# Kernel tuning notes

Measured on AMD Instinct MI355X. Metric: run time of the kernel, lower is better.

Reference implementation:

```python
import jax, jax.numpy as jnp
import numpy as np
from math import factorial as _f

# ---------- Wigner 3j / real Clebsch-Gordan (numpy, build-time) ----------

def _w3j(j1, j2, j3, m1, m2, m3):
    if m1 + m2 + m3 != 0 or not (abs(j1 - j2) <= j3 <= j1 + j2):
        return 0.0
    t1, t2 = j2 - m1 - j3, j1 + m2 - j3
    t3, t4, t5 = j1 + j2 - j3, j1 - m1, j2 + m2
    s = 0.0
    for t in range(max(0, t1, t2), min(t3, t4, t5) + 1):
        s += (-1.0) ** t / (_f(t) * _f(t - t1) * _f(t - t2) * _f(t3 - t) * _f(t4 - t) * _f(t5 - t))
    n = ((-1.0) ** (j1 - j2 - m3)
         * (_f(j1 + j2 - j3) * _f(j1 - j2 + j3) * _f(-j1 + j2 + j3) / _f(j1 + j2 + j3 + 1)) ** 0.5
         * (_f(j1 + m1) * _f(j1 - m1) * _f(j2 + m2) * _f(j2 - m2) * _f(j3 + m3) * _f(j3 - m3)) ** 0.5)
    return n * s


def _Umat(l):
    # complex -> real spherical-harmonic basis change
    U = np.zeros((2 * l + 1, 2 * l + 1), dtype=complex)
    U[l, l] = 1.0
    s2 = 1.0 / np.sqrt(2.0)
    for m in range(1, l + 1):
        U[l + m, l + m] = (-1.0) ** m * s2
        U[l + m, l - m] = s2
        U[l - m, l - m] = 1j * s2
        U[l - m, l + m] = -1j * (-1.0) ** m * s2
    return U


def _real_cg(l1, l2, l3):
    Cc = np.zeros((2 * l1 + 1, 2 * l2 + 1, 2 * l3 + 1), dtype=complex)
    for m1 in range(-l1, l1 + 1):
        for m2 in range(-l2, l2 + 1):
            m3 = m1 + m2
            if abs(m3) <= l3:
                Cc[l1 + m1, l2 + m2, l3 + m3] = ((-1.0) ** (l1 - l2 + m3) * np.sqrt(2 * l3 + 1)
                                                 * _w3j(l1, l2, l3, m1, m2, -m3))
    C = np.einsum('am,bn,co,mno->abc', _Umat(l1), _Umat(l2), np.conj(_Umat(l3)), Cc)
    C = C.imag if np.abs(C.imag).sum() > np.abs(C.real).sum() else C.real
    C = C / np.sqrt((C ** 2).sum())  # w3j normalization
    return (C * np.sqrt(2 * l3 + 1)).astype(np.float32)  # component normalization

_TRIPLES = [(1, 1, 2), (1, 2, 3), (0, 0, 0), (1, 1, 0), (2, 2, 0),
            (0, 1, 1), (1, 0, 1), (1, 2, 1), (2, 1, 1), (3, 2, 1),
            (0, 2, 2), (2, 0, 2), (2, 2, 2), (3, 1, 2)]
_CG = {k: jnp.asarray(_real_cg(*k)) for k in _TRIPLES}

# tensor-product channel lists: (l_Y, l_V) pairs producing each output l (filter 0e+1o+2e)
_P_L0 = [(0, 0), (1, 1), (2, 2)]
_P_L1 = [(0, 1), (1, 0), (1, 2), (2, 1), (3, 2)]
_P_L2 = [(0, 2), (1, 1), (2, 0), (2, 2), (3, 1)]
_EPS = 0.1       # epsilon (~1/sqrt(avg_num_neighbors))
_ENV_P = 6       # polynomial envelope order


def _sph(u):
    # component-normalized real spherical harmonics l=0..3 of unit vectors u, m=-l..l order
    E = u.shape[0]
    y0 = jnp.ones((E, 1), u.dtype)
    y1 = np.float32(np.sqrt(3.0)) * u[:, jnp.array([1, 2, 0])]  # real l=1 basis (y,z,x)
    t2 = jnp.einsum('abc,ea,eb->ec', _CG[(1, 1, 2)], y1, y1)
    y2 = t2 * (np.float32(np.sqrt(5.0)) / jnp.linalg.norm(t2, axis=-1, keepdims=True))
    t3 = jnp.einsum('abc,ea,eb->ec', _CG[(1, 2, 3)], y1, y2)
    y3 = t3 * (np.float32(np.sqrt(7.0)) / jnp.linalg.norm(t3, axis=-1, keepdims=True))
    return jnp.concatenate([y0, y1, y2, y3], axis=-1)  # (E,16)


def _lin(h, W):
    return h @ (W / np.float32(np.sqrt(W.shape[0])))  # fan-in normalized linear


def _envelope(d):
    p = _ENV_P
    c1 = np.float32((p + 1) * (p + 2) / 2.0)
    c2 = np.float32(p * (p + 2))
    c3 = np.float32(p * (p + 1) / 2.0)
    f = 1.0 - c1 * d ** p + c2 * d ** (p + 1) - c3 * d ** (p + 2)
    return jnp.where(d < 1.0, f, 0.0)


def _forward(vectors, x, V, senders, n_nodes, W1, W2a, W2b, W2c, Wv1, Wv2):
    E = vectors.shape[0]
    lengths = jnp.linalg.norm(vectors, axis=-1)            # (E,)
    Y = _sph(vectors / lengths[:, None])                   # (E,16)
    w = _lin(x, W1)                                        # (E,64) edge weights
    wY = w[:, :, None] * Y[:, None, :]                     # (E,64,16)
    node = jax.ops.segment_sum(wY, senders, num_segments=n_nodes)
    wY = node[senders] * np.float32(_EPS)                  # scatter_sum with map_back
    A = {0: wY[..., 0:1], 1: wY[..., 1:4], 2: wY[..., 4:9], 3: wY[..., 9:16]}
    B = {0: V[..., 0:1], 1: V[..., 1:4], 2: V[..., 4:9]}

    def tp(pairs, l3):
        outs = [jnp.einsum('abc,eua,eub->euc', _CG[(l1, l2, l3)], A[l1], B[l2])
                for (l1, l2) in pairs]
        return jnp.stack(outs, axis=2)                     # (E,64,n_pairs,2l3+1)

    S = tp(_P_L0, 0).reshape(E, -1)                        # (E,192) 0e scalars -> join x
    V1 = tp(_P_L1, 1).reshape(E, -1, 3)                    # (E,320,3) 1o
    V2 = tp(_P_L2, 2).reshape(E, -1, 5)                    # (E,320,5) 2e

    x2 = jnp.concatenate([x, S], axis=1)                   # (E, d_x+192)
    h = jax.nn.silu(_lin(x2, W2a))
    h = jax.nn.silu(_lin(h, W2b))
    h = _lin(h, W2c)                                       # (E,64), no output act
    x_out = _envelope(lengths)[:, None] * h                # smoothing envelope

    V1o = jnp.einsum('euc,uk->ekc', V1, Wv1 / np.float32(np.sqrt(Wv1.shape[0])))  # (E,64,3)
    V2e = jnp.einsum('euc,uk->ekc', V2, Wv2 / np.float32(np.sqrt(Wv2.shape[0])))  # (E,64,5)
    V_out = jnp.concatenate([V1o.reshape(E, -1), V2e.reshape(E, -1)], axis=1)     # (E,512)
    return x_out, V_out


def setup_inputs() -> dict:
    key = jax.random.key(0)
    ks = jax.random.split(key, 12)
    E, N, DX, MUL = 32768, 2048, 128, 64
    vectors = jax.random.uniform(ks[0], (E, 3), jnp.float32) - 0.5  # |r| < 1 (inside cutoff)
    x = jax.random.normal(ks[1], (E, DX), jnp.float32)
    V = jax.random.normal(ks[2], (E, MUL, 9), jnp.float32)          # 64 slots x (0e+1o+2e)
    senders = jax.random.randint(ks[3], (E,), 0, N)
    species = jax.random.randint(ks[4], (N,), 0, 4, jnp.int32)
    W1 = jax.random.normal(ks[5], (DX, MUL), jnp.float32)
    W2a = jax.random.normal(ks[6], (DX + 192, 64), jnp.float32)
    W2b = jax.random.normal(ks[7], (64, 64), jnp.float32)
    W2c = jax.random.normal(ks[8], (64, 64), jnp.float32)
    Wv1 = jax.random.normal(ks[9], (320, 64), jnp.float32)
    Wv2 = jax.random.normal(ks[10], (320, 64), jnp.float32)
    return dict(vectors=vectors, x=x, V=V, senders=senders, species=species,
                W1=W1, W2a=W2a, W2b=W2b, W2c=W2c, Wv1=Wv1, Wv2=Wv2)


def reference(vectors, x, V, senders, species, W1, W2a, W2b, W2c, Wv1, Wv2):
    # species is unused by the layer body (matches original signature)
    return _forward(vectors, x, V, senders, int(species.shape[0]), W1, W2a, W2b, W2c, Wv1, Wv2)
```

## Files before the change

kernel.cpp:

```cpp
#include <hip/hip_runtime.h>
#include <cmath>
#include <complex>
#include <vector>
#include <algorithm>

namespace {

static double factd(int n) { double r = 1; for (int i = 2; i <= n; i++) r *= i; return r; }
static double par(int k) { return (k % 2 == 0) ? 1.0 : -1.0; }

static double w3j(int j1, int j2, int j3, int m1, int m2, int m3) {
    if (m1 + m2 + m3 != 0) return 0.0;
    if (j3 < std::abs(j1 - j2) || j3 > j1 + j2) return 0.0;
    int t1 = j2 - m1 - j3, t2 = j1 + m2 - j3;
    int t3 = j1 + j2 - j3, t4 = j1 - m1, t5 = j2 + m2;
    int lo = std::max(0, std::max(t1, t2)), hi = std::min(t3, std::min(t4, t5));
    double s = 0.0;
    for (int t = lo; t <= hi; t++)
        s += par(t) / (factd(t) * factd(t - t1) * factd(t - t2) *
                       factd(t3 - t) * factd(t4 - t) * factd(t5 - t));
    double n = par(j1 - j2 - m3)
        * std::sqrt(factd(j1 + j2 - j3) * factd(j1 - j2 + j3) * factd(-j1 + j2 + j3) / factd(j1 + j2 + j3 + 1))
        * std::sqrt(factd(j1 + m1) * factd(j1 - m1) * factd(j2 + m2) * factd(j2 - m2) * factd(j3 + m3) * factd(j3 - m3));
    return n * s;
}

static void Umat(int l, std::complex<double>* U) {
    int n = 2 * l + 1;
    for (int i = 0; i < n * n; i++) U[i] = 0.0;
    U[l * n + l] = 1.0;
    double s2 = 1.0 / std::sqrt(2.0);
    for (int m = 1; m <= l; m++) {
        U[(l + m) * n + (l + m)] = par(m) * s2;
        U[(l + m) * n + (l - m)] = s2;
        U[(l - m) * n + (l - m)] = std::complex<double>(0.0, s2);
        U[(l - m) * n + (l + m)] = std::complex<double>(0.0, -par(m) * s2);
    }
}

static void real_cg(int l1, int l2, int l3, float* out) {
    int n1 = 2 * l1 + 1, n2 = 2 * l2 + 1, n3 = 2 * l3 + 1;
    std::vector<std::complex<double>> Cc((size_t)n1 * n2 * n3, 0.0);
    for (int m1 = -l1; m1 <= l1; m1++)
        for (int m2 = -l2; m2 <= l2; m2++) {
            int m3 = m1 + m2;
            if (std::abs(m3) <= l3)
                Cc[((size_t)(l1 + m1) * n2 + (l2 + m2)) * n3 + (l3 + m3)] =
                    par(l1 - l2 + m3) * std::sqrt((double)(2 * l3 + 1)) * w3j(l1, l2, l3, m1, m2, -m3);
        }
    std::vector<std::complex<double>> U1((size_t)n1 * n1), U2((size_t)n2 * n2), U3((size_t)n3 * n3);
    Umat(l1, U1.data()); Umat(l2, U2.data()); Umat(l3, U3.data());
    std::vector<std::complex<double>> C((size_t)n1 * n2 * n3, 0.0);
    for (int a = 0; a < n1; a++)
        for (int b = 0; b < n2; b++)
            for (int c = 0; c < n3; c++) {
                std::complex<double> s = 0.0;
                for (int m = 0; m < n1; m++)
                    for (int nn = 0; nn < n2; nn++) {
                        std::complex<double> u12 = U1[(size_t)a * n1 + m] * U2[(size_t)b * n2 + nn];
                        if (u12 == std::complex<double>(0.0, 0.0)) continue;
                        for (int o = 0; o < n3; o++) {
                            std::complex<double> cc = Cc[((size_t)m * n2 + nn) * n3 + o];
                            if (cc == std::complex<double>(0.0, 0.0)) continue;
                            s += u12 * std::conj(U3[(size_t)c * n3 + o]) * cc;
                        }
                    }
                C[((size_t)a * n2 + b) * n3 + c] = s;
            }
    double sim = 0, sre = 0;
    for (auto& z : C) { sim += std::abs(z.imag()); sre += std::abs(z.real()); }
    std::vector<double> R(C.size());
    for (size_t i = 0; i < C.size(); i++) R[i] = (sim > sre) ? C[i].imag() : C[i].real();
    double ss = 0; for (double v : R) ss += v * v;
    double scale = std::sqrt((double)(2 * l3 + 1)) / std::sqrt(ss);
    for (size_t i = 0; i < R.size(); i++) out[i] = (float)(R[i] * scale);
}

}

struct CGPack {
    float c000[1];  float c110[9];   float c220[25];
    float c011[9];  float c101[9];   float c121[45];  float c211[45]; float c321[105];
    float c022[25]; float c202[25];  float c222[125]; float c312[105];
    float c112[45]; float c123[105];
};

static void build_pack(CGPack& p) {
    real_cg(0, 0, 0, p.c000); real_cg(1, 1, 0, p.c110); real_cg(2, 2, 0, p.c220);
    real_cg(0, 1, 1, p.c011); real_cg(1, 0, 1, p.c101); real_cg(1, 2, 1, p.c121);
    real_cg(2, 1, 1, p.c211); real_cg(3, 2, 1, p.c321);
    real_cg(0, 2, 2, p.c022); real_cg(2, 0, 2, p.c202); real_cg(2, 2, 2, p.c222);
    real_cg(3, 1, 2, p.c312); real_cg(1, 1, 2, p.c112); real_cg(1, 2, 3, p.c123);
}


template <int NA, int NB, int NC>
__device__ __forceinline__ void tpc(const float* __restrict__ C,
                                    const float* __restrict__ a,
                                    const float* __restrict__ b,
                                    float* __restrict__ out) {
#pragma unroll
    for (int c = 0; c < NC; c++) {
        float s = 0.f;
#pragma unroll
        for (int i = 0; i < NA; i++) {
#pragma unroll
            for (int j = 0; j < NB; j++)
                s += C[(i * NB + j) * NC + c] * a[i] * b[j];
        }
        out[c] = s;
    }
}

__device__ __forceinline__ float silu(float v) { return v / (1.f + expf(-v)); }

#define EPSC 0.1f
#define INV_SQRT128 0.08838834764831845f
#define INV_SQRT320 0.05590169943749474f
#define SQRT5 2.2360679774997896f
#define SQRT7 2.6457513110645907f
#define SQRT3 1.7320508075688772f

__global__ __launch_bounds__(256) void k_edge_pre(
    const float* __restrict__ vectors, const float* __restrict__ x,
    const int* __restrict__ senders, const float* __restrict__ W1,
    float* __restrict__ node, int E, CGPack cg) {
    int wid = (blockIdx.x * blockDim.x + threadIdx.x) >> 6;
    int lane = threadIdx.x & 63;
    if (wid >= E) return;
    int e = wid;
    float vx = vectors[e * 3 + 0], vy = vectors[e * 3 + 1], vz = vectors[e * 3 + 2];
    float inv = rsqrtf(vx * vx + vy * vy + vz * vz);
    float ux = vx * inv, uy = vy * inv, uz = vz * inv;

    float Y[16];
    Y[0] = 1.f;
    float y1[3] = { SQRT3 * uy, SQRT3 * uz, SQRT3 * ux };
    float t2[5]; tpc<3, 3, 5>(cg.c112, y1, y1, t2);
    float n2 = 0.f;
#pragma unroll
    for (int c = 0; c < 5; c++) n2 += t2[c] * t2[c];
    float sc2 = SQRT5 * rsqrtf(n2);
    float y2[5];
#pragma unroll
    for (int c = 0; c < 5; c++) y2[c] = t2[c] * sc2;
    float t3[7]; tpc<3, 5, 7>(cg.c123, y1, y2, t3);
    float n3 = 0.f;
#pragma unroll
    for (int c = 0; c < 7; c++) n3 += t3[c] * t3[c];
    float sc3 = SQRT7 * rsqrtf(n3);
#pragma unroll
    for (int j = 0; j < 3; j++) Y[1 + j] = y1[j];
#pragma unroll
    for (int j = 0; j < 5; j++) Y[4 + j] = y2[j];
#pragma unroll
    for (int j = 0; j < 7; j++) Y[9 + j] = t3[j] * sc3;

    const float* xr = x + (size_t)e * 128;
    float w = 0.f;
#pragma unroll 4
    for (int d = 0; d < 128; d++) w += xr[d] * W1[d * 64 + lane];
    w *= INV_SQRT128;

    int s = senders[e];
    float* nb = node + (size_t)s * 1024 + lane;
#pragma unroll
    for (int k = 0; k < 16; k++) atomicAdd(nb + k * 64, w * Y[k]);
}

__global__ __launch_bounds__(64) void k_edge_main(
    const float* __restrict__ vectors, const float* __restrict__ x,
    const float* __restrict__ V, const int* __restrict__ senders,
    const float* __restrict__ node,
    const float* __restrict__ W2a, const float* __restrict__ W2b, const float* __restrict__ W2c,
    const float* __restrict__ Wv1, const float* __restrict__ Wv2,
    float* __restrict__ xout, float* __restrict__ vout, int E, CGPack cg) {
    __shared__ float Ssh[192];
    __shared__ float V1sh[320 * 3];
    __shared__ float V2sh[320 * 5];
    __shared__ float Hsh[64];

    int e = blockIdx.x;
    int u = threadIdx.x;
    int s = senders[e];

    const float* nb = node + (size_t)s * 1024 + u;
    float a0 = nb[0] * EPSC;
    float a1[3], a2[5], a3[7];
#pragma unroll
    for (int j = 0; j < 3; j++) a1[j] = nb[(1 + j) * 64] * EPSC;
#pragma unroll
    for (int j = 0; j < 5; j++) a2[j] = nb[(4 + j) * 64] * EPSC;
#pragma unroll
    for (int j = 0; j < 7; j++) a3[j] = nb[(9 + j) * 64] * EPSC;

    const float* vb = V + (size_t)e * 576 + u * 9;
    float b0 = vb[0];
    float b1[3] = { vb[1], vb[2], vb[3] };
    float b2[5] = { vb[4], vb[5], vb[6], vb[7], vb[8] };

    {
        float o[1];
        Ssh[u * 3 + 0] = cg.c000[0] * a0 * b0;
        tpc<3, 3, 1>(cg.c110, a1, b1, o); Ssh[u * 3 + 1] = o[0];
        tpc<5, 5, 1>(cg.c220, a2, b2, o); Ssh[u * 3 + 2] = o[0];
    }
    {
        float* v1 = V1sh + u * 15;
        tpc<1, 3, 3>(cg.c011, &a0, b1, v1 + 0);
        tpc<3, 1, 3>(cg.c101, a1, &b0, v1 + 3);
        tpc<3, 5, 3>(cg.c121, a1, b2, v1 + 6);
        tpc<5, 3, 3>(cg.c211, a2, b1, v1 + 9);
        tpc<7, 5, 3>(cg.c321, a3, b2, v1 + 12);
    }
    {
        float* v2 = V2sh + u * 25;
        tpc<1, 5, 5>(cg.c022, &a0, b2, v2 + 0);
        tpc<3, 3, 5>(cg.c112, a1, b1, v2 + 5);
        tpc<5, 1, 5>(cg.c202, a2, &b0, v2 + 10);
        tpc<5, 5, 5>(cg.c222, a2, b2, v2 + 15);
        tpc<7, 3, 5>(cg.c312, a3, b1, v2 + 20);
    }
    __syncthreads();

    const float* xr = x + (size_t)e * 128;
    float h = 0.f;
    for (int d = 0; d < 128; d++) h += xr[d] * W2a[d * 64 + u];
    for (int j = 0; j < 192; j++) h += Ssh[j] * W2a[(128 + j) * 64 + u];
    h = silu(h * INV_SQRT320);
    Hsh[u] = h;
    __syncthreads();
    float h2 = 0.f;
    for (int j = 0; j < 64; j++) h2 += Hsh[j] * W2b[j * 64 + u];
    h2 = silu(h2 * 0.125f);
    __syncthreads();
    Hsh[u] = h2;
    __syncthreads();
    float h3 = 0.f;
    for (int j = 0; j < 64; j++) h3 += Hsh[j] * W2c[j * 64 + u];
    h3 *= 0.125f;

    float vx = vectors[e * 3 + 0], vy = vectors[e * 3 + 1], vz = vectors[e * 3 + 2];
    float len = sqrtf(vx * vx + vy * vy + vz * vz);
    float d2 = len * len, d4 = d2 * d2, d6 = d4 * d2, d7 = d6 * len, d8 = d7 * len;
    float env = 1.f - 28.f * d6 + 48.f * d7 - 21.f * d8;
    if (!(len < 1.f)) env = 0.f;
    xout[(size_t)e * 64 + u] = env * h3;

    float acc1[3] = { 0.f, 0.f, 0.f };
    for (int t = 0; t < 320; t++) {
        float wv = Wv1[t * 64 + u];
        acc1[0] += V1sh[t * 3 + 0] * wv;
        acc1[1] += V1sh[t * 3 + 1] * wv;
        acc1[2] += V1sh[t * 3 + 2] * wv;
    }
    float* vo = vout + (size_t)e * 512;
#pragma unroll
    for (int c = 0; c < 3; c++) vo[u * 3 + c] = acc1[c] * INV_SQRT320;

    float acc2[5] = { 0.f, 0.f, 0.f, 0.f, 0.f };
    for (int t = 0; t < 320; t++) {
        float wv = Wv2[t * 64 + u];
#pragma unroll
        for (int c = 0; c < 5; c++) acc2[c] += V2sh[t * 5 + c] * wv;
    }
#pragma unroll
    for (int c = 0; c < 5; c++) vo[192 + u * 5 + c] = acc2[c] * INV_SQRT320;
}

extern "C" void kernel_launch(void* const* d_in, const int* in_sizes, int n_in,
                              void* d_out, int out_size, void* d_ws, size_t ws_size,
                              hipStream_t stream) {
    const float* vectors = (const float*)d_in[0];
    const float* x       = (const float*)d_in[1];
    const float* V       = (const float*)d_in[2];
    const int*   senders = (const int*)d_in[3];
    const float* W1  = (const float*)d_in[5];
    const float* W2a = (const float*)d_in[6];
    const float* W2b = (const float*)d_in[7];
    const float* W2c = (const float*)d_in[8];
    const float* Wv1 = (const float*)d_in[9];
    const float* Wv2 = (const float*)d_in[10];

    int E = in_sizes[0] / 3;
    int N = in_sizes[4];

    CGPack pack;
    build_pack(pack);

    float* node = (float*)d_ws;
    hipMemsetAsync(node, 0, (size_t)N * 1024 * sizeof(float), stream);

    dim3 blkA(256), grdA((unsigned)(((size_t)E * 64 + 255) / 256));
    hipLaunchKernelGGL(k_edge_pre, grdA, blkA, 0, stream,
                       vectors, x, senders, W1, node, E, pack);

    float* xout = (float*)d_out;
    float* vout = xout + (size_t)E * 64;
    hipLaunchKernelGGL(k_edge_main, dim3((unsigned)E), dim3(64), 0, stream,
                       vectors, x, V, senders, node,
                       W2a, W2b, W2c, Wv1, Wv2, xout, vout, E, pack);
}
```

Before: 793.1 us.

## Process two edges per block and transpose shared tensor-product buffers for float4 reads

Each block of k_edge_main now handles two edges with 128 threads instead of one edge with 64. The V1/V2 tensor-product intermediates are stored component-major in shared memory so the weight contraction can read float4 vectors. The two separate 320-step loops over Wv1 and Wv2 are fused into one loop unrolled by 4. This is meant to cut per-block launch and sync overhead and the shared-memory and global-load instruction count. In exchange it uses more shared memory per block and assumes E is divisible by 2.

Result: slower. 1.099 ms (+38.6%).

```diff
diff --git a/kernel.cpp b/kernel.cpp
--- a/kernel.cpp
+++ b/kernel.cpp
@@ -168,20 +168,22 @@
     for (int k = 0; k < 16; k++) atomicAdd(nb + k * 64, w * Y[k]);
 }
 
-__global__ __launch_bounds__(64) void k_edge_main(
+#define EPB 2
+__global__ __launch_bounds__(128) void k_edge_main(
     const float* __restrict__ vectors, const float* __restrict__ x,
     const float* __restrict__ V, const int* __restrict__ senders,
     const float* __restrict__ node,
     const float* __restrict__ W2a, const float* __restrict__ W2b, const float* __restrict__ W2c,
     const float* __restrict__ Wv1, const float* __restrict__ Wv2,
     float* __restrict__ xout, float* __restrict__ vout, int E, CGPack cg) {
-    __shared__ float Ssh[192];
-    __shared__ float V1sh[320 * 3];
-    __shared__ float V2sh[320 * 5];
-    __shared__ float Hsh[64];
-
-    int e = blockIdx.x;
-    int u = threadIdx.x;
+    __shared__ __align__(16) float V1sh[EPB][3][320];
+    __shared__ __align__(16) float V2sh[EPB][5][320];
+    __shared__ float Ssh[EPB][192];
+    __shared__ float Hsh[EPB][64];
+
+    int eo = threadIdx.x >> 6;
+    int u  = threadIdx.x & 63;
+    int e  = blockIdx.x * EPB + eo;
     int s = senders[e];
 
     const float* nb = node + (size_t)s * 1024 + u;
@@ -201,43 +203,51 @@
 
     {
         float o[1];
-        Ssh[u * 3 + 0] = cg.c000[0] * a0 * b0;
-        tpc<3, 3, 1>(cg.c110, a1, b1, o); Ssh[u * 3 + 1] = o[0];
-        tpc<5, 5, 1>(cg.c220, a2, b2, o); Ssh[u * 3 + 2] = o[0];
+        Ssh[eo][u * 3 + 0] = cg.c000[0] * a0 * b0;
+        tpc<3, 3, 1>(cg.c110, a1, b1, o); Ssh[eo][u * 3 + 1] = o[0];
+        tpc<5, 5, 1>(cg.c220, a2, b2, o); Ssh[eo][u * 3 + 2] = o[0];
     }
     {
-        float* v1 = V1sh + u * 15;
-        tpc<1, 3, 3>(cg.c011, &a0, b1, v1 + 0);
-        tpc<3, 1, 3>(cg.c101, a1, &b0, v1 + 3);
-        tpc<3, 5, 3>(cg.c121, a1, b2, v1 + 6);
-        tpc<5, 3, 3>(cg.c211, a2, b1, v1 + 9);
-        tpc<7, 5, 3>(cg.c321, a3, b2, v1 + 12);
+        float v1t[5][3];
+        tpc<1, 3, 3>(cg.c011, &a0, b1, v1t[0]);
+        tpc<3, 1, 3>(cg.c101, a1, &b0, v1t[1]);
+        tpc<3, 5, 3>(cg.c121, a1, b2, v1t[2]);
+        tpc<5, 3, 3>(cg.c211, a2, b1, v1t[3]);
+        tpc<7, 5, 3>(cg.c321, a3, b2, v1t[4]);
+#pragma unroll
+        for (int p = 0; p < 5; p++)
+#pragma unroll
+            for (int c = 0; c < 3; c++) V1sh[eo][c][u * 5 + p] = v1t[p][c];
     }
     {
-        float* v2 = V2sh + u * 25;
-        tpc<1, 5, 5>(cg.c022, &a0, b2, v2 + 0);
-        tpc<3, 3, 5>(cg.c112, a1, b1, v2 + 5);
-        tpc<5, 1, 5>(cg.c202, a2, &b0, v2 + 10);
-        tpc<5, 5, 5>(cg.c222, a2, b2, v2 + 15);
-        tpc<7, 3, 5>(cg.c312, a3, b1, v2 + 20);
+        float v2t[5][5];
+        tpc<1, 5, 5>(cg.c022, &a0, b2, v2t[0]);
+        tpc<3, 3, 5>(cg.c112, a1, b1, v2t[1]);
+        tpc<5, 1, 5>(cg.c202, a2, &b0, v2t[2]);
+        tpc<5, 5, 5>(cg.c222, a2, b2, v2t[3]);
+        tpc<7, 3, 5>(cg.c312, a3, b1, v2t[4]);
+#pragma unroll
+        for (int p = 0; p < 5; p++)
+#pragma unroll
+            for (int c = 0; c < 5; c++) V2sh[eo][c][u * 5 + p] = v2t[p][c];
     }
     __syncthreads();
 
     const float* xr = x + (size_t)e * 128;
     float h = 0.f;
     for (int d = 0; d < 128; d++) h += xr[d] * W2a[d * 64 + u];
-    for (int j = 0; j < 192; j++) h += Ssh[j] * W2a[(128 + j) * 64 + u];
+    for (int j = 0; j < 192; j++) h += Ssh[eo][j] * W2a[(128 + j) * 64 + u];
     h = silu(h * INV_SQRT320);
-    Hsh[u] = h;
+    Hsh[eo][u] = h;
     __syncthreads();
     float h2 = 0.f;
-    for (int j = 0; j < 64; j++) h2 += Hsh[j] * W2b[j * 64 + u];
+    for (int j = 0; j < 64; j++) h2 += Hsh[eo][j] * W2b[j * 64 + u];
     h2 = silu(h2 * 0.125f);
     __syncthreads();
-    Hsh[u] = h2;
+    Hsh[eo][u] = h2;
     __syncthreads();
     float h3 = 0.f;
-    for (int j = 0; j < 64; j++) h3 += Hsh[j] * W2c[j * 64 + u];
+    for (int j = 0; j < 64; j++) h3 += Hsh[eo][j] * W2c[j * 64 + u];
     h3 *= 0.125f;
 
     float vx = vectors[e * 3 + 0], vy = vectors[e * 3 + 1], vz = vectors[e * 3 + 2];
@@ -248,22 +258,29 @@
     xout[(size_t)e * 64 + u] = env * h3;
 
     float acc1[3] = { 0.f, 0.f, 0.f };
-    for (int t = 0; t < 320; t++) {
-        float wv = Wv1[t * 64 + u];
-        acc1[0] += V1sh[t * 3 + 0] * wv;
-        acc1[1] += V1sh[t * 3 + 1] * wv;
-        acc1[2] += V1sh[t * 3 + 2] * wv;
+    float acc2[5] = { 0.f, 0.f, 0.f, 0.f, 0.f };
+    const float* wv1p = Wv1 + u;
+    const float* wv2p = Wv2 + u;
+    for (int t4 = 0; t4 < 80; ++t4) {
+        int t = t4 * 4;
+        float w10 = wv1p[(t + 0) * 64], w11 = wv1p[(t + 1) * 64];
+        float w12 = wv1p[(t + 2) * 64], w13 = wv1p[(t + 3) * 64];
+        float w20 = wv2p[(t + 0) * 64], w21 = wv2p[(t + 1) * 64];
+        float w22 = wv2p[(t + 2) * 64], w23 = wv2p[(t + 3) * 64];
+#pragma unroll
+        for (int c = 0; c < 3; c++) {
+            float4 v = *(const float4*)&V1sh[eo][c][t];
+            acc1[c] += v.x * w10 + v.y * w11 + v.z * w12 + v.w * w13;
+        }
+#pragma unroll
+        for (int c = 0; c < 5; c++) {
+            float4 v = *(const float4*)&V2sh[eo][c][t];
+            acc2[c] += v.x * w20 + v.y * w21 + v.z * w22 + v.w * w23;
+        }
     }
     float* vo = vout + (size_t)e * 512;
 #pragma unroll
     for (int c = 0; c < 3; c++) vo[u * 3 + c] = acc1[c] * INV_SQRT320;
-
-    float acc2[5] = { 0.f, 0.f, 0.f, 0.f, 0.f };
-    for (int t = 0; t < 320; t++) {
-        float wv = Wv2[t * 64 + u];
-#pragma unroll
-        for (int c = 0; c < 5; c++) acc2[c] += V2sh[t * 5 + c] * wv;
-    }
 #pragma unroll
     for (int c = 0; c < 5; c++) vo[192 + u * 5 + c] = acc2[c] * INV_SQRT320;
 }
@@ -297,7 +314,7 @@
 
     float* xout = (float*)d_out;
     float* vout = xout + (size_t)E * 64;
-    hipLaunchKernelGGL(k_edge_main, dim3((unsigned)E), dim3(64), 0, stream,
+    hipLaunchKernelGGL(k_edge_main, dim3((unsigned)(E / EPB)), dim3(64 * EPB), 0, stream,
                        vectors, x, V, senders, node,
                        W2a, W2b, W2c, Wv1, Wv2, xout, vout, E, pack);
 }
```

## Transpose V1/V2 shared buffers and fuse Wv1/Wv2 loops with interleaved weights

Applied to the files above, without the earlier changes.

Stores the l=1 and l=2 tensor-product intermediates component-major in shared memory so the output projection can read them as float4 vectors. A small pre-kernel interleaves Wv1 and Wv2 into a float2 array in workspace so one load feeds both projections, and the two 320-step loops are merged into one loop unrolled by four. Adds an occupancy hint to launch bounds. The cost is an extra kernel launch and workspace use, plus strided shared stores in the tensor-product phase.

Result: faster. 747.9 us (-5.7%).

```diff
diff --git a/kernel.cpp b/kernel.cpp
--- a/kernel.cpp
+++ b/kernel.cpp
@@ -112,6 +112,24 @@
     }
 }
 
+template <int NA, int NB, int NC, int ST>
+__device__ __forceinline__ void tpcs(const float* __restrict__ C,
+                                     const float* __restrict__ a,
+                                     const float* __restrict__ b,
+                                     float* __restrict__ out) {
+#pragma unroll
+    for (int c = 0; c < NC; c++) {
+        float s = 0.f;
+#pragma unroll
+        for (int i = 0; i < NA; i++) {
+#pragma unroll
+            for (int j = 0; j < NB; j++)
+                s += C[(i * NB + j) * NC + c] * a[i] * b[j];
+        }
+        out[c * ST] = s;
+    }
+}
+
 __device__ __forceinline__ float silu(float v) { return v / (1.f + expf(-v)); }
 
 #define EPSC 0.1f
@@ -120,6 +138,13 @@
 #define SQRT5 2.2360679774997896f
 #define SQRT7 2.6457513110645907f
 #define SQRT3 1.7320508075688772f
+
+__global__ __launch_bounds__(256) void k_fuse_wv(
+    const float* __restrict__ Wv1, const float* __restrict__ Wv2,
+    float2* __restrict__ WvI) {
+    int i = blockIdx.x * blockDim.x + threadIdx.x;
+    if (i < 320 * 64) WvI[i] = make_float2(Wv1[i], Wv2[i]);
+}
 
 __global__ __launch_bounds__(256) void k_edge_pre(
     const float* __restrict__ vectors, const float* __restrict__ x,
@@ -168,16 +193,15 @@
     for (int k = 0; k < 16; k++) atomicAdd(nb + k * 64, w * Y[k]);
 }
 
-__global__ __launch_bounds__(64) void k_edge_main(
+__global__ __launch_bounds__(64, 4) void k_edge_main(
     const float* __restrict__ vectors, const float* __restrict__ x,
     const float* __restrict__ V, const int* __restrict__ senders,
-    const float* __restrict__ node,
+    const float* __restrict__ node, const float2* __restrict__ WvI,
     const float* __restrict__ W2a, const float* __restrict__ W2b, const float* __restrict__ W2c,
-    const float* __restrict__ Wv1, const float* __restrict__ Wv2,
     float* __restrict__ xout, float* __restrict__ vout, int E, CGPack cg) {
+    __shared__ __align__(16) float V1sh[3][320];
+    __shared__ __align__(16) float V2sh[5][320];
     __shared__ float Ssh[192];
-    __shared__ float V1sh[320 * 3];
-    __shared__ float V2sh[320 * 5];
     __shared__ float Hsh[64];
 
     int e = blockIdx.x;
@@ -206,20 +230,20 @@
         tpc<5, 5, 1>(cg.c220, a2, b2, o); Ssh[u * 3 + 2] = o[0];
     }
     {
-        float* v1 = V1sh + u * 15;
-        tpc<1, 3, 3>(cg.c011, &a0, b1, v1 + 0);
-        tpc<3, 1, 3>(cg.c101, a1, &b0, v1 + 3);
-        tpc<3, 5, 3>(cg.c121, a1, b2, v1 + 6);
-        tpc<5, 3, 3>(cg.c211, a2, b1, v1 + 9);
-        tpc<7, 5, 3>(cg.c321, a3, b2, v1 + 12);
+        float* v1 = &V1sh[0][u * 5];
+        tpcs<1, 3, 3, 320>(cg.c011, &a0, b1, v1 + 0);
+        tpcs<3, 1, 3, 320>(cg.c101, a1, &b0, v1 + 1);
+        tpcs<3, 5, 3, 320>(cg.c121, a1, b2, v1 + 2);
+        tpcs<5, 3, 3, 320>(cg.c211, a2, b1, v1 + 3);
+        tpcs<7, 5, 3, 320>(cg.c321, a3, b2, v1 + 4);
     }
     {
-        float* v2 = V2sh + u * 25;
-        tpc<1, 5, 5>(cg.c022, &a0, b2, v2 + 0);
-        tpc<3, 3, 5>(cg.c112, a1, b1, v2 + 5);
-        tpc<5, 1, 5>(cg.c202, a2, &b0, v2 + 10);
-        tpc<5, 5, 5>(cg.c222, a2, b2, v2 + 15);
-        tpc<7, 3, 5>(cg.c312, a3, b1, v2 + 20);
+        float* v2 = &V2sh[0][u * 5];
+        tpcs<1, 5, 5, 320>(cg.c022, &a0, b2, v2 + 0);
+        tpcs<3, 3, 5, 320>(cg.c112, a1, b1, v2 + 1);
+        tpcs<5, 1, 5, 320>(cg.c202, a2, &b0, v2 + 2);
+        tpcs<5, 5, 5, 320>(cg.c222, a2, b2, v2 + 3);
+        tpcs<7, 3, 5, 320>(cg.c312, a3, b1, v2 + 4);
     }
     __syncthreads();
 
@@ -248,22 +272,28 @@
     xout[(size_t)e * 64 + u] = env * h3;
 
     float acc1[3] = { 0.f, 0.f, 0.f };
-    for (int t = 0; t < 320; t++) {
-        float wv = Wv1[t * 64 + u];
-        acc1[0] += V1sh[t * 3 + 0] * wv;
-        acc1[1] += V1sh[t * 3 + 1] * wv;
-        acc1[2] += V1sh[t * 3 + 2] * wv;
+    float acc2[5] = { 0.f, 0.f, 0.f, 0.f, 0.f };
+    const float2* wvp = WvI + u;
+    for (int t4 = 0; t4 < 80; ++t4) {
+        int t = t4 * 4;
+        float2 w0 = wvp[(t + 0) * 64];
+        float2 w1 = wvp[(t + 1) * 64];
+        float2 w2 = wvp[(t + 2) * 64];
+        float2 w3 = wvp[(t + 3) * 64];
+#pragma unroll
+        for (int c = 0; c < 3; c++) {
+            float4 v = *(const float4*)&V1sh[c][t];
+            acc1[c] += v.x * w0.x + v.y * w1.x + v.z * w2.x + v.w * w3.x;
+        }
+#pragma unroll
+        for (int c = 0; c < 5; c++) {
+            float4 v = *(const float4*)&V2sh[c][t];
+            acc2[c] += v.x * w0.y + v.y * w1.y + v.z * w2.y + v.w * w3.y;
+        }
     }
     float* vo = vout + (size_t)e * 512;
 #pragma unroll
     for (int c = 0; c < 3; c++) vo[u * 3 + c] = acc1[c] * INV_SQRT320;
-
-    float acc2[5] = { 0.f, 0.f, 0.f, 0.f, 0.f };
-    for (int t = 0; t < 320; t++) {
-        float wv = Wv2[t * 64 + u];
-#pragma unroll
-        for (int c = 0; c < 5; c++) acc2[c] += V2sh[t * 5 + c] * wv;
-    }
 #pragma unroll
     for (int c = 0; c < 5; c++) vo[192 + u * 5 + c] = acc2[c] * INV_SQRT320;
 }
@@ -288,8 +318,12 @@
     CGPack pack;
     build_pack(pack);
 
-    float* node = (float*)d_ws;
+    float*  node = (float*)d_ws;
+    float2* WvI  = (float2*)((char*)d_ws + (size_t)N * 1024 * sizeof(float));
     hipMemsetAsync(node, 0, (size_t)N * 1024 * sizeof(float), stream);
+
+    hipLaunchKernelGGL(k_fuse_wv, dim3((320 * 64 + 255) / 256), dim3(256), 0, stream,
+                       Wv1, Wv2, WvI);
 
     dim3 blkA(256), grdA((unsigned)(((size_t)E * 64 + 255) / 256));
     hipLaunchKernelGGL(k_edge_pre, grdA, blkA, 0, stream,
@@ -298,6 +332,6 @@
     float* xout = (float*)d_out;
     float* vout = xout + (size_t)E * 64;
     hipLaunchKernelGGL(k_edge_main, dim3((unsigned)E), dim3(64), 0, stream,
-                       vectors, x, V, senders, node,
-                       W2a, W2b, W2c, Wv1, Wv2, xout, vout, E, pack);
-}
+                       vectors, x, V, senders, node, WvI,
+                       W2a, W2b, W2c, xout, vout, E, pack);
+}
```
